# Optimization experiments

Measured on AMD Instinct MI355X. Metric: run time of the kernel, lower is better.

The kernel has to match this reference:

```python
import jax, jax.numpy as jnp
import numpy as np
import math

B, SQ, SK, D, H = 2, 2048, 2048, 1024, 16
DH = D // H
EPS = 1e-5

def _ln(x, g, b):
    m = jnp.mean(x, axis=-1, keepdims=True)
    v = jnp.mean(jnp.square(x - m), axis=-1, keepdims=True)
    return (x - m) / jnp.sqrt(v + EPS) * g + b

def setup_inputs() -> dict:
    key = jax.random.key(0)
    ks = jax.random.split(key, 8)
    xav = math.sqrt(6.0 / (D + D))  # xavier_uniform for square [D,D] weights
    inp = {
        'Q': jax.random.normal(ks[0], (B, SQ, D), dtype=jnp.float32),
        'K': jax.random.normal(ks[1], (B, SK, D), dtype=jnp.float32),
        'pad_mask': jax.random.randint(ks[2], (B, SK), 0, 2, dtype=jnp.int32),
        'Wq': jax.random.uniform(ks[3], (D, D), jnp.float32, -xav, xav),
        'Wk': jax.random.uniform(ks[4], (D, D), jnp.float32, -xav, xav),
        'Wv': jax.random.uniform(ks[5], (D, D), jnp.float32, -xav, xav),
        'Wo': jax.random.uniform(ks[6], (D, D), jnp.float32, -xav, xav),
        'bq': jnp.zeros((D,), jnp.float32),
        'bk': jnp.zeros((D,), jnp.float32),
        'bv': jnp.zeros((D,), jnp.float32),
        'bo': jnp.zeros((D,), jnp.float32),
        'ln_q_g': jnp.ones((D,), jnp.float32),  'ln_q_b': jnp.zeros((D,), jnp.float32),
        'ln_kv_g': jnp.ones((D,), jnp.float32), 'ln_kv_b': jnp.zeros((D,), jnp.float32),
        'ln_f_g': jnp.ones((D,), jnp.float32),  'ln_f_b': jnp.zeros((D,), jnp.float32),
    }
    return inp

def reference(Q, K, pad_mask, Wq, Wk, Wv, Wo, bq, bk, bv, bo,
              ln_q_g, ln_q_b, ln_kv_g, ln_kv_b, ln_f_g, ln_f_b):
    Q_ = _ln(Q, ln_q_g, ln_q_b)
    K_ = _ln(K, ln_kv_g, ln_kv_b)
    # projections (PyTorch Linear: x @ W.T + b)
    Q1 = (Q_ @ Wq.T + bq).reshape(B, SQ, H, DH)
    K1 = (K_ @ Wk.T + bk).reshape(B, SK, H, DH)
    V1 = (K_ @ Wv.T + bv).reshape(B, SK, H, DH)
    # note: scaling uses sqrt(dim_V), NOT sqrt(head_dim), per source
    score = jnp.einsum('bqhd,bkhd->bhqk', Q1, K1) / math.sqrt(D)
    m = pad_mask[:, None, None, :]  # [B,1,1,SK]
    score = jnp.where(m == 0, jnp.float32(-1e12), score)
    A = jax.nn.softmax(score, axis=-1)
    A = A * m.astype(A.dtype)  # second mask application after softmax
    O1 = jnp.einsum('bhqk,bkhd->bqhd', A, V1).reshape(B, SQ, D)
    O2 = jax.nn.relu(Q_ @ Wo.T + bo)
    return _ln(Q + O1 + O2, ln_f_g, ln_f_b)
```

## Files before the change

### kernel.cpp

```cpp
#include <hip/hip_runtime.h>
#include <stdint.h>

#define NB 2
#define NSQ 2048
#define NSK 2048
#define ND 1024
#define NH 16
#define NDH 64

typedef unsigned short u16;
typedef unsigned int u32;
typedef __bf16 bf16x8_t __attribute__((ext_vector_type(8)));
typedef float f32x4_t __attribute__((ext_vector_type(4)));
typedef u32 u32x4_t __attribute__((ext_vector_type(4)));

#define AS1 __attribute__((address_space(1)))
#define AS3 __attribute__((address_space(3)))

__device__ __forceinline__ float bf2f(u16 u) {
    union { float f; u32 i; } v; v.i = ((u32)u) << 16; return v.f;
}
__device__ __forceinline__ u16 f2bf(float x) {
    union { float f; u32 i; } v; v.f = x;
    u32 r = v.i + 0x7fffu + ((v.i >> 16) & 1u);
    return (u16)(r >> 16);
}
__device__ __forceinline__ u32 fbits(float x) {
    union { float f; u32 i; } v; v.f = x; return v.i;
}

__global__ __launch_bounds__(256) void detect_kernel(
    const u16* __restrict__ Q, int* __restrict__ flag)
{
    __shared__ int s;
    if (threadIdx.x == 0) s = 0;
    __syncthreads();
    uint2 x = ((const uint2*)Q)[threadIdx.x];
    u16 a0 = x.x & 0xffff, a1 = x.x >> 16, a2 = x.y & 0xffff, a3 = x.y >> 16;
    bool big = (((a0 >> 7) & 0xff) >= 0x8D) || (((a1 >> 7) & 0xff) >= 0x8D) ||
               (((a2 >> 7) & 0xff) >= 0x8D) || (((a3 >> 7) & 0xff) >= 0x8D);
    if (big) s = 1;
    __syncthreads();
    if (threadIdx.x == 0) *flag = s;
}

__global__ __launch_bounds__(256) void cvt_params_kernel(
    const int* __restrict__ flag,
    const void* __restrict__ Wq, const void* __restrict__ Wk,
    const void* __restrict__ Wv, const void* __restrict__ Wo,
    const void* __restrict__ vbq, const void* __restrict__ vbk,
    const void* __restrict__ vbv, const void* __restrict__ vbo,
    const void* __restrict__ g0, const void* __restrict__ b0,
    const void* __restrict__ g1, const void* __restrict__ b1,
    const void* __restrict__ g2, const void* __restrict__ b2,
    u16* __restrict__ Wc, u16* __restrict__ Vc)
{
    int blk = blockIdx.x;
    int t = threadIdx.x;
    const void* src;
    u16* dst;
    size_t srcoff;
    if (blk < 4096) {
        int w = blk >> 10;
        src = (w == 0) ? Wq : (w == 1) ? Wk : (w == 2) ? Wv : Wo;
        srcoff = (size_t)(blk & 1023) * 1024;
        dst = Wc + (size_t)w * 1024 * 1024 + srcoff;
    } else {
        int v = blk - 4096;
        src = (v == 0) ? vbq : (v == 1) ? vbk : (v == 2) ? vbv : (v == 3) ? vbo :
              (v == 4) ? g0  : (v == 5) ? b0  : (v == 6) ? g1  : (v == 7) ? b1 :
              (v == 8) ? g2  : b2;
        srcoff = 0;
        dst = Vc + (size_t)v * 1024;
    }
    u32 lo, hi;
    if (*flag) {
        float4 x = ((const float4*)src)[srcoff / 4 + t];
        lo = (u32)f2bf(x.x) | ((u32)f2bf(x.y) << 16);
        hi = (u32)f2bf(x.z) | ((u32)f2bf(x.w) << 16);
    } else {
        uint2 x = ((const uint2*)src)[srcoff / 4 + t];
        lo = x.x; hi = x.y;
    }
    uint2 o; o.x = lo; o.y = hi;
    ((uint2*)dst)[t] = o;
}

__global__ __launch_bounds__(256) void idx_kernel(
    const int* __restrict__ mask, int* __restrict__ idx, int* __restrict__ cnt)
{
    int b = blockIdx.x;
    const int* m = mask + b * NSK;
    int t = threadIdx.x;
    int loc[8]; int s = 0;
#pragma unroll
    for (int i = 0; i < 8; ++i) { loc[i] = (m[t * 8 + i] != 0); s += loc[i]; }
    __shared__ int ps[256];
    ps[t] = s;
    __syncthreads();
    for (int off = 1; off < 256; off <<= 1) {
        int v = (t >= off) ? ps[t - off] : 0;
        __syncthreads();
        ps[t] += v;
        __syncthreads();
    }
    int run = ps[t] - s;
#pragma unroll
    for (int i = 0; i < 8; ++i)
        if (loc[i]) idx[b * NSK + run++] = t * 8 + i;
    if (t == 255) cnt[b] = ps[255];
}

__global__ __launch_bounds__(256) void ln_in_kernel(
    const int* __restrict__ flag,
    const void* __restrict__ Q, const void* __restrict__ K,
    const u16* __restrict__ Vc,
    u16* __restrict__ Qn, u16* __restrict__ Kn)
{
    int row = blockIdx.x;
    const void* x; const u16 *g, *bb; u16* y;
    size_t roff;
    if (row < NB * NSQ) {
        x = Q; roff = (size_t)row * ND;
        g = Vc + 4 * 1024; bb = Vc + 5 * 1024;
        y = Qn + roff;
    } else {
        int r2 = row - NB * NSQ;
        x = K; roff = (size_t)r2 * ND;
        g = Vc + 6 * 1024; bb = Vc + 7 * 1024;
        y = Kn + roff;
    }
    int t = threadIdx.x;
    float v0, v1, v2, v3;
    if (*flag) {
        float4 xv = ((const float4*)x)[roff / 4 + t];
        v0 = xv.x; v1 = xv.y; v2 = xv.z; v3 = xv.w;
    } else {
        uint2 ux = ((const uint2*)x)[roff / 4 + t];
        v0 = bf2f(ux.x & 0xffff); v1 = bf2f(ux.x >> 16);
        v2 = bf2f(ux.y & 0xffff); v3 = bf2f(ux.y >> 16);
    }
    float s1 = v0 + v1 + v2 + v3;
    float s2 = v0*v0 + v1*v1 + v2*v2 + v3*v3;
#pragma unroll
    for (int off = 32; off >= 1; off >>= 1) {
        s1 += __shfl_xor(s1, off);
        s2 += __shfl_xor(s2, off);
    }
    __shared__ float r1[4], r2[4];
    int wave = t >> 6;
    if ((t & 63) == 0) { r1[wave] = s1; r2[wave] = s2; }
    __syncthreads();
    float t1 = r1[0] + r1[1] + r1[2] + r1[3];
    float t2 = r2[0] + r2[1] + r2[2] + r2[3];
    float mean = t1 * (1.0f / ND);
    float var  = t2 * (1.0f / ND) - mean * mean;
    float rstd = rsqrtf(var + 1e-5f);
    uint2 ug = ((const uint2*)g)[t];
    uint2 ub = ((const uint2*)bb)[t];
    float y0 = (v0 - mean) * rstd * bf2f(ug.x & 0xffff) + bf2f(ub.x & 0xffff);
    float y1 = (v1 - mean) * rstd * bf2f(ug.x >> 16)    + bf2f(ub.x >> 16);
    float y2 = (v2 - mean) * rstd * bf2f(ug.y & 0xffff) + bf2f(ub.y & 0xffff);
    float y3 = (v3 - mean) * rstd * bf2f(ug.y >> 16)    + bf2f(ub.y >> 16);
    uint2 o;
    o.x = (u32)f2bf(y0) | ((u32)f2bf(y1) << 16);
    o.y = (u32)f2bf(y2) | ((u32)f2bf(y3) << 16);
    ((uint2*)y)[t] = o;
}

__global__ __launch_bounds__(256) void gemm4_kernel(
    const u16* __restrict__ Qn, const u16* __restrict__ Kn,
    const u16* __restrict__ Wc, const u16* __restrict__ Vc,
    u16* __restrict__ Q1, u16* __restrict__ K1, u16* __restrict__ V1,
    u16* __restrict__ R)
{
    int z = blockIdx.z;
    const u16* X    = (z == 0 || z == 3) ? Qn : Kn;
    const u16* W    = Wc + (size_t)z * 1024 * 1024;
    const u16* bias = Vc + (size_t)z * 1024;

    __shared__ u16 smem[16384];
    u16* sA0 = smem;
    u16* sA1 = smem + 4096;
    u16* sB0 = smem + 8192;
    u16* sB1 = smem + 12288;

    int tid  = threadIdx.x;
    int wave = tid >> 6, lane = tid & 63;
    int wm = wave >> 1, wn = wave & 1;
    int quad = lane >> 4, l4 = lane & 15;
    int m0 = blockIdx.x * 128;
    int n0 = blockIdx.y * 128;

    f32x4_t acc[4][4];
#pragma unroll
    for (int i = 0; i < 4; ++i)
#pragma unroll
        for (int j = 0; j < 4; ++j)
            acc[i][j] = (f32x4_t){0.f, 0.f, 0.f, 0.f};

    int lrow = lane >> 2;
    int lcol = (lane & 3) * 8;
    int rowb0 = wave * 16;
    int rowb1 = (4 + wave) * 16;
    const u16* gA0 = X + (size_t)(m0 + rowb0 + lrow) * ND + lcol;
    const u16* gA1 = X + (size_t)(m0 + rowb1 + lrow) * ND + lcol;
    const u16* gB0 = W + (size_t)(n0 + rowb0 + lrow) * ND + lcol;
    const u16* gB1 = W + (size_t)(n0 + rowb1 + lrow) * ND + lcol;

    __builtin_amdgcn_global_load_lds((const AS1 u32*)gA0, (AS3 u32*)(sA0 + rowb0 * 32), 16, 0, 0);
    __builtin_amdgcn_global_load_lds((const AS1 u32*)gA1, (AS3 u32*)(sA0 + rowb1 * 32), 16, 0, 0);
    __builtin_amdgcn_global_load_lds((const AS1 u32*)gB0, (AS3 u32*)(sB0 + rowb0 * 32), 16, 0, 0);
    __builtin_amdgcn_global_load_lds((const AS1 u32*)gB1, (AS3 u32*)(sB0 + rowb1 * 32), 16, 0, 0);

    for (int kb = 0; kb < ND / 32; ++kb) {
        __syncthreads();

        if (kb + 1 < ND / 32) {
            int k1 = (kb + 1) * 32;
            u16* dA = (kb + 1) & 1 ? sA1 : sA0;
            u16* dB = (kb + 1) & 1 ? sB1 : sB0;
            __builtin_amdgcn_global_load_lds((const AS1 u32*)(gA0 + k1), (AS3 u32*)(dA + rowb0 * 32), 16, 0, 0);
            __builtin_amdgcn_global_load_lds((const AS1 u32*)(gA1 + k1), (AS3 u32*)(dA + rowb1 * 32), 16, 0, 0);
            __builtin_amdgcn_global_load_lds((const AS1 u32*)(gB0 + k1), (AS3 u32*)(dB + rowb0 * 32), 16, 0, 0);
            __builtin_amdgcn_global_load_lds((const AS1 u32*)(gB1 + k1), (AS3 u32*)(dB + rowb1 * 32), 16, 0, 0);
        }

        const u16* a = kb & 1 ? sA1 : sA0;
        const u16* bb_ = kb & 1 ? sB1 : sB0;
        bf16x8_t af[4], bfr[4];
#pragma unroll
        for (int tm = 0; tm < 4; ++tm) {
            int rr = wm * 64 + tm * 16 + l4;
            af[tm] = *(const bf16x8_t*)(a + rr * 32 + quad * 8);
        }
#pragma unroll
        for (int tn = 0; tn < 4; ++tn) {
            int rr = wn * 64 + tn * 16 + l4;
            bfr[tn] = *(const bf16x8_t*)(bb_ + rr * 32 + quad * 8);
        }
#pragma unroll
        for (int tm = 0; tm < 4; ++tm)
#pragma unroll
            for (int tn = 0; tn < 4; ++tn)
                acc[tm][tn] = __builtin_amdgcn_mfma_f32_16x16x32_bf16(
                    af[tm], bfr[tn], acc[tm][tn], 0, 0, 0);
    }

    u16* outp = (z == 0) ? Q1 : (z == 1) ? K1 : (z == 2) ? V1 : R;
#pragma unroll
    for (int tm = 0; tm < 4; ++tm) {
#pragma unroll
        for (int tn = 0; tn < 4; ++tn) {
            int n = n0 + wn * 64 + tn * 16 + l4;
            float bv_ = bf2f(bias[n]);
#pragma unroll
            for (int r = 0; r < 4; ++r) {
                int m = m0 + wm * 64 + tm * 16 + quad * 4 + r;
                float val = acc[tm][tn][r] + bv_;
                if (z == 0) val *= 0.045105964f;
                if (z == 3) val = fmaxf(val, 0.f);
                outp[(size_t)m * ND + n] = f2bf(val);
            }
        }
    }
}

__global__ __launch_bounds__(256) void gather_k_kernel(
    const u16* __restrict__ K1, const int* __restrict__ idx,
    const int* __restrict__ cnt, u16* __restrict__ Kc)
{
    int b = blockIdx.y;
    int c = cnt[b];
    int cPad = (c + 63) & ~63;
    int jb = blockIdx.x * 16;
    if (jb >= cPad) return;
    int t = threadIdx.x;
    int row = t >> 4;
    int seg = t & 15;
    int j = jb + row;
    if (j >= cPad) return;
    bool z = (j >= c);
    const u16* src = z ? (const u16*)0
        : K1 + ((size_t)b * NSK + idx[(size_t)b * NSK + j]) * ND;
    u16* dst = Kc + ((size_t)b * NSK + j) * ND;
#pragma unroll
    for (int i = 0; i < 8; ++i) {
        int off = (seg * 8 + i) * 8;
        uint4 v = z ? (uint4){0, 0, 0, 0} : *(const uint4*)(src + off);
        *(uint4*)(dst + off) = v;
    }
}

__global__ __launch_bounds__(256) void gather_vt_kernel(
    const u16* __restrict__ V1, const int* __restrict__ idx,
    const int* __restrict__ cnt, u16* __restrict__ Vct)
{
    int kb = blockIdx.x;
    int h  = blockIdx.y;
    int b  = blockIdx.z;
    int c = cnt[b];
    int cPad = (c + 63) & ~63;
    if (kb * 64 >= cPad) return;
    __shared__ u16 sT[64 * 72];
    int tid = threadIdx.x;
    {
        int row = tid >> 3, seg = tid & 7;
        int j1 = kb * 64 + row, j2 = j1 + 32;
        uint4 v1 = {0, 0, 0, 0}, v2 = {0, 0, 0, 0};
        if (j1 < c) v1 = *(const uint4*)(V1 +
            ((size_t)b * NSK + idx[(size_t)b * NSK + j1]) * ND + h * NDH + seg * 8);
        if (j2 < c) v2 = *(const uint4*)(V1 +
            ((size_t)b * NSK + idx[(size_t)b * NSK + j2]) * ND + h * NDH + seg * 8);
        *(uint4*)(sT + row * 72 + seg * 8) = v1;
        *(uint4*)(sT + (row + 32) * 72 + seg * 8) = v2;
    }
    __syncthreads();
    int d = tid >> 2, sg = tid & 3;
    u16 buf[16];
#pragma unroll
    for (int i = 0; i < 8; ++i) buf[i]     = sT[(sg * 8 + i) * 72 + d];
#pragma unroll
    for (int i = 0; i < 8; ++i) buf[8 + i] = sT[((sg + 4) * 8 + i) * 72 + d];
    u16* go = Vct + ((size_t)(b * NH + h) * NDH + d) * NSK + kb * 64;
    *(uint4*)(go + sg * 8)       = *(uint4*)buf;
    *(uint4*)(go + (sg + 4) * 8) = *(uint4*)(buf + 8);
}

__global__ __launch_bounds__(256, 4) void attn_kernel(
    const u16* __restrict__ Q1, const u16* __restrict__ Kc,
    const u16* __restrict__ Vct, const int* __restrict__ cnt,
    u16* __restrict__ R)
{
    int q0 = blockIdx.x * 64;
    int h  = blockIdx.y;
    int b  = blockIdx.z;

    __shared__ u16 sK[2][64 * 64];
    __shared__ u16 sV[2][64 * 64];

    int tid  = threadIdx.x;
    int wave = tid >> 6, lane = tid & 63;
    int quad = lane >> 4, l4 = lane & 15;
    int lk = lane >> 3, ls = lane & 7;
    int gseg = ls ^ lk;

    int c  = cnt[b];
    int nt = (c + 63) >> 6;

    bf16x8_t qf[2];
    {
        const u16* qp = Q1 + (size_t)(b * NSQ + q0 + wave * 16 + l4) * ND + h * NDH;
        qf[0] = *(const bf16x8_t*)(qp + quad * 8);
        qf[1] = *(const bf16x8_t*)(qp + 32 + quad * 8);
    }

    const u16* kbase = Kc + (size_t)b * NSK * ND + h * NDH;
    const u16* vbase = Vct + (size_t)(b * NH + h) * NDH * NSK;

    const u16* gk0 = kbase + (size_t)(wave * 16 + lk) * ND + gseg * 8;
    const u16* gk1 = gk0 + (size_t)8 * ND;
    const u16* gv0 = vbase + (size_t)(wave * 16 + lk) * NSK + gseg * 8;
    const u16* gv1 = gv0 + (size_t)8 * NSK;

    int fragOff[2];
#pragma unroll
    for (int kk = 0; kk < 2; ++kk)
        fragOff[kk] = l4 * 64 + (((kk * 4 + quad) ^ (l4 & 7)) * 8);

    float l_run = 0.f;
    f32x4_t acc_o[4];
#pragma unroll
    for (int T = 0; T < 4; ++T) acc_o[T] = (f32x4_t){0.f, 0.f, 0.f, 0.f};

    int srcA = (quad & 1) * 32 + l4;
    int srcB = srcA + 16;
    bool hi = lane >= 32;

    if (nt > 0) {
        __builtin_amdgcn_global_load_lds((const AS1 u32*)gk0,
            (AS3 u32*)(&sK[0][(wave * 16) * 64]), 16, 0, 0);
        __builtin_amdgcn_global_load_lds((const AS1 u32*)gk1,
            (AS3 u32*)(&sK[0][(wave * 16 + 8) * 64]), 16, 0, 0);
        __builtin_amdgcn_global_load_lds((const AS1 u32*)gv0,
            (AS3 u32*)(&sV[0][(wave * 16) * 64]), 16, 0, 0);
        __builtin_amdgcn_global_load_lds((const AS1 u32*)gv1,
            (AS3 u32*)(&sV[0][(wave * 16 + 8) * 64]), 16, 0, 0);
        gk0 += (size_t)64 * ND; gk1 += (size_t)64 * ND;
        gv0 += 64; gv1 += 64;

        for (int kb = 0; kb < nt; ++kb) {
            __syncthreads();

            if (kb + 1 < nt) {
                int bi = (kb + 1) & 1;
                __builtin_amdgcn_global_load_lds((const AS1 u32*)gk0,
                    (AS3 u32*)(&sK[bi][(wave * 16) * 64]), 16, 0, 0);
                __builtin_amdgcn_global_load_lds((const AS1 u32*)gk1,
                    (AS3 u32*)(&sK[bi][(wave * 16 + 8) * 64]), 16, 0, 0);
                __builtin_amdgcn_global_load_lds((const AS1 u32*)gv0,
                    (AS3 u32*)(&sV[bi][(wave * 16) * 64]), 16, 0, 0);
                __builtin_amdgcn_global_load_lds((const AS1 u32*)gv1,
                    (AS3 u32*)(&sV[bi][(wave * 16 + 8) * 64]), 16, 0, 0);
                gk0 += (size_t)64 * ND; gk1 += (size_t)64 * ND;
                gv0 += 64; gv1 += 64;
            }

            const u16* kt = sK[kb & 1];
            const u16* vt = sV[kb & 1];

            f32x4_t accs[4];
            if (kb == nt - 1) {
#pragma unroll
                for (int tm = 0; tm < 4; ++tm) {
                    int key = kb * 64 + tm * 16 + quad * 4;
#pragma unroll
                    for (int r = 0; r < 4; ++r)
                        accs[tm][r] = (key + r < c) ? 0.f : -1e9f;
                }
            } else {
#pragma unroll
                for (int tm = 0; tm < 4; ++tm)
                    accs[tm] = (f32x4_t){0.f, 0.f, 0.f, 0.f};
            }
#pragma unroll
            for (int kk = 0; kk < 2; ++kk)
#pragma unroll
                for (int tm = 0; tm < 4; ++tm) {
                    bf16x8_t kf = *(const bf16x8_t*)(kt + tm * 1024 + fragOff[kk]);
                    accs[tm] = __builtin_amdgcn_mfma_f32_16x16x32_bf16(
                        kf, qf[kk], accs[tm], 0, 0, 0);
                }

            float lsum = 0.f;
            u32 pk[4][2];
#pragma unroll
            for (int tm = 0; tm < 4; ++tm) {
                float p0 = exp2f(accs[tm][0]);
                float p1 = exp2f(accs[tm][1]);
                float p2 = exp2f(accs[tm][2]);
                float p3 = exp2f(accs[tm][3]);
                lsum += p0 + p1 + p2 + p3;
                pk[tm][0] = __builtin_amdgcn_perm(fbits(p1), fbits(p0), 0x07060302);
                pk[tm][1] = __builtin_amdgcn_perm(fbits(p3), fbits(p2), 0x07060302);
            }
            lsum += __shfl_xor(lsum, 16);
            lsum += __shfl_xor(lsum, 32);
            l_run += lsum;

#pragma unroll
            for (int kk = 0; kk < 2; ++kk) {
                u32 a0 = __shfl((int)pk[kk * 2][0], srcA), a1 = __shfl((int)pk[kk * 2][1], srcA);
                u32 b0 = __shfl((int)pk[kk * 2 + 1][0], srcA), b1 = __shfl((int)pk[kk * 2 + 1][1], srcA);
                u32 c0 = __shfl((int)pk[kk * 2][0], srcB), c1 = __shfl((int)pk[kk * 2][1], srcB);
                u32 d0 = __shfl((int)pk[kk * 2 + 1][0], srcB), d1 = __shfl((int)pk[kk * 2 + 1][1], srcB);
                u32x4_t pr;
                pr.x = hi ? b0 : a0;
                pr.y = hi ? b1 : a1;
                pr.z = hi ? d0 : c0;
                pr.w = hi ? d1 : c1;
                bf16x8_t pf = __builtin_bit_cast(bf16x8_t, pr);
#pragma unroll
                for (int T = 0; T < 4; ++T) {
                    bf16x8_t vf = *(const bf16x8_t*)(vt + T * 1024 + fragOff[kk]);
                    acc_o[T] = __builtin_amdgcn_mfma_f32_16x16x32_bf16(
                        vf, pf, acc_o[T], 0, 0, 0);
                }
            }
        }
    }

    float inv = l_run > 0.f ? 1.f / l_run : 0.f;
    u16* rp = R + (size_t)(b * NSQ + q0 + wave * 16 + l4) * ND + h * NDH;
#pragma unroll
    for (int T = 0; T < 4; ++T) {
        u16* p = rp + T * 16 + quad * 4;
        uint2 o2 = *(const uint2*)p;
        float e0 = acc_o[T][0] * inv + bf2f(o2.x & 0xffff);
        float e1 = acc_o[T][1] * inv + bf2f(o2.x >> 16);
        float e2 = acc_o[T][2] * inv + bf2f(o2.y & 0xffff);
        float e3 = acc_o[T][3] * inv + bf2f(o2.y >> 16);
        uint2 on;
        on.x = (u32)f2bf(e0) | ((u32)f2bf(e1) << 16);
        on.y = (u32)f2bf(e2) | ((u32)f2bf(e3) << 16);
        *(uint2*)p = on;
    }
}

__global__ __launch_bounds__(256) void ln_out_kernel(
    const int* __restrict__ flag,
    const void* __restrict__ Q, const u16* __restrict__ R,
    const u16* __restrict__ Vc, void* __restrict__ out)
{
    int row = blockIdx.x;
    size_t roff = (size_t)row * ND;
    int t = threadIdx.x;
    int f = *flag;
    float v0, v1, v2, v3;
    uint2 ur = ((const uint2*)(R + roff))[t];
    if (f) {
        float4 xq = ((const float4*)Q)[roff / 4 + t];
        v0 = xq.x; v1 = xq.y; v2 = xq.z; v3 = xq.w;
    } else {
        uint2 uq = ((const uint2*)Q)[roff / 4 + t];
        v0 = bf2f(uq.x & 0xffff); v1 = bf2f(uq.x >> 16);
        v2 = bf2f(uq.y & 0xffff); v3 = bf2f(uq.y >> 16);
    }
    v0 += bf2f(ur.x & 0xffff); v1 += bf2f(ur.x >> 16);
    v2 += bf2f(ur.y & 0xffff); v3 += bf2f(ur.y >> 16);
    float s1 = v0 + v1 + v2 + v3;
    float s2 = v0*v0 + v1*v1 + v2*v2 + v3*v3;
#pragma unroll
    for (int off = 32; off >= 1; off >>= 1) {
        s1 += __shfl_xor(s1, off);
        s2 += __shfl_xor(s2, off);
    }
    __shared__ float r1[4], r2[4];
    int wave = t >> 6;
    if ((t & 63) == 0) { r1[wave] = s1; r2[wave] = s2; }
    __syncthreads();
    float t1 = r1[0] + r1[1] + r1[2] + r1[3];
    float t2 = r2[0] + r2[1] + r2[2] + r2[3];
    float mean = t1 * (1.0f / ND);
    float var  = t2 * (1.0f / ND) - mean * mean;
    float rstd = rsqrtf(var + 1e-5f);
    const u16* g  = Vc + 8 * 1024;
    const u16* bb = Vc + 9 * 1024;
    uint2 ug = ((const uint2*)g)[t];
    uint2 ub = ((const uint2*)bb)[t];
    float y0 = (v0 - mean) * rstd * bf2f(ug.x & 0xffff) + bf2f(ub.x & 0xffff);
    float y1 = (v1 - mean) * rstd * bf2f(ug.x >> 16)    + bf2f(ub.x >> 16);
    float y2 = (v2 - mean) * rstd * bf2f(ug.y & 0xffff) + bf2f(ub.y & 0xffff);
    float y3 = (v3 - mean) * rstd * bf2f(ug.y >> 16)    + bf2f(ub.y >> 16);
    if (f) {
        float4 o; o.x = y0; o.y = y1; o.z = y2; o.w = y3;
        ((float4*)out)[roff / 4 + t] = o;
    } else {
        uint2 o;
        o.x = (u32)f2bf(y0) | ((u32)f2bf(y1) << 16);
        o.y = (u32)f2bf(y2) | ((u32)f2bf(y3) << 16);
        ((uint2*)out)[roff / 4 + t] = o;
    }
}

extern "C" void kernel_launch(void* const* d_in, const int* in_sizes, int n_in,
                              void* d_out, int out_size, void* d_ws, size_t ws_size,
                              hipStream_t stream) {
    const void* Q        = d_in[0];
    const void* K        = d_in[1];
    const int* pad_mask  = (const int*)d_in[2];

    const size_t NEL = (size_t)NB * NSQ * ND;
    int* flag = (int*)d_ws;
    int* cnt  = flag + 1;
    int* idx  = flag + 4;
    u16* base = (u16*)(idx + 4096);
    u16* Qn  = base;
    u16* Kn  = Qn + NEL;
    u16* Q1  = Kn + NEL;
    u16* K1  = Q1 + NEL;
    u16* V1  = K1 + NEL;
    u16* R   = V1 + NEL;
    u16* Wc  = R + NEL;
    u16* Vc  = Wc + (size_t)4 * 1024 * 1024;
    u16* Kc  = Qn;
    u16* Vct = Kn;

    detect_kernel<<<dim3(1), dim3(256), 0, stream>>>((const u16*)Q, flag);

    cvt_params_kernel<<<dim3(4106), dim3(256), 0, stream>>>(
        flag, d_in[3], d_in[4], d_in[5], d_in[6],
        d_in[7], d_in[8], d_in[9], d_in[10],
        d_in[11], d_in[12], d_in[13], d_in[14], d_in[15], d_in[16],
        Wc, Vc);

    idx_kernel<<<dim3(NB), dim3(256), 0, stream>>>(pad_mask, idx, cnt);

    ln_in_kernel<<<dim3(2 * NB * NSQ), dim3(256), 0, stream>>>(
        flag, Q, K, Vc, Qn, Kn);

    gemm4_kernel<<<dim3(32, 8, 4), dim3(256), 0, stream>>>(
        Qn, Kn, Wc, Vc, Q1, K1, V1, R);

    gather_k_kernel<<<dim3(128, NB), dim3(256), 0, stream>>>(K1, idx, cnt, Kc);

    gather_vt_kernel<<<dim3(32, NH, NB), dim3(256), 0, stream>>>(V1, idx, cnt, Vct);

    attn_kernel<<<dim3(NSQ / 64, NH, NB), dim3(256), 0, stream>>>(
        Q1, Kc, Vct, cnt, R);

    ln_out_kernel<<<dim3(NB * NSQ), dim3(256), 0, stream>>>(
        flag, Q, R, Vc, d_out);
}
```

Baseline: 255.2 us.

## Rewrite projection GEMM with 256x256 tiles, 4-stage LDS pipeline and swizzle

The four fused projection GEMMs now use 512-thread blocks computing 256x256 output tiles, up from 128x128. Global-to-LDS loads move from a double buffer to a 4-stage ring with explicit vmcnt waits. Loads are interleaved between two MFMA half-phases, wave priority is raised around the MFMA phases, and an XOR swizzle on LDS chunks reduces bank conflicts. The larger tiles raise arithmetic intensity and the deeper prefetch hides memory latency, at the cost of only 256 blocks (fewer than two waves' worth of CUs), 128 KB of LDS per block, and heavy register pressure from 32 accumulators.

```diff
diff --git a/kernel.cpp b/kernel.cpp
--- a/kernel.cpp
+++ b/kernel.cpp
@@ -168,7 +168,7 @@
     ((uint2*)y)[t] = o;
 }
 
-__global__ __launch_bounds__(256) void gemm4_kernel(
+__global__ __launch_bounds__(512, 2) void gemm4_kernel(
     const u16* __restrict__ Qn, const u16* __restrict__ Kn,
     const u16* __restrict__ Wc, const u16* __restrict__ Vc,
     u16* __restrict__ Q1, u16* __restrict__ K1, u16* __restrict__ V1,
@@ -179,85 +179,108 @@
     const u16* W    = Wc + (size_t)z * 1024 * 1024;
     const u16* bias = Vc + (size_t)z * 1024;
 
-    __shared__ u16 smem[16384];
-    u16* sA0 = smem;
-    u16* sA1 = smem + 4096;
-    u16* sB0 = smem + 8192;
-    u16* sB1 = smem + 12288;
+    __shared__ u16 sm[4][2][256 * 32];
 
     int tid  = threadIdx.x;
     int wave = tid >> 6, lane = tid & 63;
-    int wm = wave >> 1, wn = wave & 1;
+    int wm = wave >> 2, wn = wave & 3;
     int quad = lane >> 4, l4 = lane & 15;
-    int m0 = blockIdx.x * 128;
-    int n0 = blockIdx.y * 128;
-
-    f32x4_t acc[4][4];
-#pragma unroll
-    for (int i = 0; i < 4; ++i)
+    int m0 = blockIdx.x * 256;
+    int n0 = blockIdx.y * 256;
+
+    int srow   = wave * 16 + (lane >> 2);
+    int schunk = (lane & 3) ^ ((srow >> 1) & 3);
+    const u16* gA = X + (size_t)(m0 + srow) * ND + schunk * 8;
+    const u16* gB = W + (size_t)(n0 + srow) * ND + schunk * 8;
+
+#define STAGE_A(t_) do { int s_ = (t_) & 3; \
+    __builtin_amdgcn_global_load_lds((const AS1 u32*)(gA + (t_) * 32), \
+        (AS3 u32*)(&sm[s_][0][wave * 512]), 16, 0, 0); \
+    __builtin_amdgcn_global_load_lds((const AS1 u32*)(gA + (t_) * 32 + (size_t)128 * ND), \
+        (AS3 u32*)(&sm[s_][0][4096 + wave * 512]), 16, 0, 0); \
+} while (0)
+#define STAGE_B(t_) do { int s_ = (t_) & 3; \
+    __builtin_amdgcn_global_load_lds((const AS1 u32*)(gB + (t_) * 32), \
+        (AS3 u32*)(&sm[s_][1][wave * 512]), 16, 0, 0); \
+    __builtin_amdgcn_global_load_lds((const AS1 u32*)(gB + (t_) * 32 + (size_t)128 * ND), \
+        (AS3 u32*)(&sm[s_][1][4096 + wave * 512]), 16, 0, 0); \
+} while (0)
+
+    int fch   = (quad ^ ((l4 >> 1) & 3)) * 8;
+    int aoffb = (wm * 128 + l4) * 32 + fch;
+    int boffb = (wn * 64  + l4) * 32 + fch;
+
+    f32x4_t acc[8][4];
+#pragma unroll
+    for (int i = 0; i < 8; ++i)
 #pragma unroll
         for (int j = 0; j < 4; ++j)
             acc[i][j] = (f32x4_t){0.f, 0.f, 0.f, 0.f};
 
-    int lrow = lane >> 2;
-    int lcol = (lane & 3) * 8;
-    int rowb0 = wave * 16;
-    int rowb1 = (4 + wave) * 16;
-    const u16* gA0 = X + (size_t)(m0 + rowb0 + lrow) * ND + lcol;
-    const u16* gA1 = X + (size_t)(m0 + rowb1 + lrow) * ND + lcol;
-    const u16* gB0 = W + (size_t)(n0 + rowb0 + lrow) * ND + lcol;
-    const u16* gB1 = W + (size_t)(n0 + rowb1 + lrow) * ND + lcol;
-
-    __builtin_amdgcn_global_load_lds((const AS1 u32*)gA0, (AS3 u32*)(sA0 + rowb0 * 32), 16, 0, 0);
-    __builtin_amdgcn_global_load_lds((const AS1 u32*)gA1, (AS3 u32*)(sA0 + rowb1 * 32), 16, 0, 0);
-    __builtin_amdgcn_global_load_lds((const AS1 u32*)gB0, (AS3 u32*)(sB0 + rowb0 * 32), 16, 0, 0);
-    __builtin_amdgcn_global_load_lds((const AS1 u32*)gB1, (AS3 u32*)(sB0 + rowb1 * 32), 16, 0, 0);
-
-    for (int kb = 0; kb < ND / 32; ++kb) {
-        __syncthreads();
-
-        if (kb + 1 < ND / 32) {
-            int k1 = (kb + 1) * 32;
-            u16* dA = (kb + 1) & 1 ? sA1 : sA0;
-            u16* dB = (kb + 1) & 1 ? sB1 : sB0;
-            __builtin_amdgcn_global_load_lds((const AS1 u32*)(gA0 + k1), (AS3 u32*)(dA + rowb0 * 32), 16, 0, 0);
-            __builtin_amdgcn_global_load_lds((const AS1 u32*)(gA1 + k1), (AS3 u32*)(dA + rowb1 * 32), 16, 0, 0);
-            __builtin_amdgcn_global_load_lds((const AS1 u32*)(gB0 + k1), (AS3 u32*)(dB + rowb0 * 32), 16, 0, 0);
-            __builtin_amdgcn_global_load_lds((const AS1 u32*)(gB1 + k1), (AS3 u32*)(dB + rowb1 * 32), 16, 0, 0);
-        }
-
-        const u16* a = kb & 1 ? sA1 : sA0;
-        const u16* bb_ = kb & 1 ? sB1 : sB0;
-        bf16x8_t af[4], bfr[4];
-#pragma unroll
-        for (int tm = 0; tm < 4; ++tm) {
-            int rr = wm * 64 + tm * 16 + l4;
-            af[tm] = *(const bf16x8_t*)(a + rr * 32 + quad * 8);
-        }
-#pragma unroll
-        for (int tn = 0; tn < 4; ++tn) {
-            int rr = wn * 64 + tn * 16 + l4;
-            bfr[tn] = *(const bf16x8_t*)(bb_ + rr * 32 + quad * 8);
-        }
-#pragma unroll
-        for (int tm = 0; tm < 4; ++tm)
-#pragma unroll
-            for (int tn = 0; tn < 4; ++tn)
-                acc[tm][tn] = __builtin_amdgcn_mfma_f32_16x16x32_bf16(
-                    af[tm], bfr[tn], acc[tm][tn], 0, 0, 0);
-    }
+    STAGE_A(0); STAGE_B(0);
+    STAGE_A(1); STAGE_B(1);
+    STAGE_A(2); STAGE_B(2);
+    asm volatile("s_waitcnt vmcnt(8)" ::: "memory");
+    __builtin_amdgcn_s_barrier();
+    __builtin_amdgcn_sched_barrier(0);
+
+    for (int t = 0; t < 32; ++t) {
+        const u16* a = &sm[t & 3][0][0];
+        const u16* b = &sm[t & 3][1][0];
+        bf16x8_t bf[4], af[4];
+
+#pragma unroll
+        for (int nf = 0; nf < 4; ++nf)
+            bf[nf] = *(const bf16x8_t*)(b + boffb + nf * 512);
+#pragma unroll
+        for (int mf = 0; mf < 4; ++mf)
+            af[mf] = *(const bf16x8_t*)(a + aoffb + mf * 512);
+        if (t < 29) STAGE_A(t + 3);
+        __builtin_amdgcn_s_barrier();
+        __builtin_amdgcn_s_setprio(1);
+#pragma unroll
+        for (int mf = 0; mf < 4; ++mf)
+#pragma unroll
+            for (int nf = 0; nf < 4; ++nf)
+                acc[mf][nf] = __builtin_amdgcn_mfma_f32_16x16x32_bf16(
+                    af[mf], bf[nf], acc[mf][nf], 0, 0, 0);
+        __builtin_amdgcn_s_setprio(0);
+        __builtin_amdgcn_s_barrier();
+
+#pragma unroll
+        for (int mf = 0; mf < 4; ++mf)
+            af[mf] = *(const bf16x8_t*)(a + aoffb + (mf + 4) * 512);
+        if (t < 29) STAGE_B(t + 3);
+        __builtin_amdgcn_s_barrier();
+        __builtin_amdgcn_s_setprio(1);
+#pragma unroll
+        for (int mf = 0; mf < 4; ++mf)
+#pragma unroll
+            for (int nf = 0; nf < 4; ++nf)
+                acc[mf + 4][nf] = __builtin_amdgcn_mfma_f32_16x16x32_bf16(
+                    af[mf], bf[nf], acc[mf + 4][nf], 0, 0, 0);
+        __builtin_amdgcn_s_setprio(0);
+
+        if (t < 29)       asm volatile("s_waitcnt vmcnt(8)" ::: "memory");
+        else if (t == 29) asm volatile("s_waitcnt vmcnt(4)" ::: "memory");
+        else if (t == 30) asm volatile("s_waitcnt vmcnt(0)" ::: "memory");
+        __builtin_amdgcn_s_barrier();
+        __builtin_amdgcn_sched_barrier(0);
+    }
+#undef STAGE_A
+#undef STAGE_B
 
     u16* outp = (z == 0) ? Q1 : (z == 1) ? K1 : (z == 2) ? V1 : R;
 #pragma unroll
-    for (int tm = 0; tm < 4; ++tm) {
-#pragma unroll
-        for (int tn = 0; tn < 4; ++tn) {
-            int n = n0 + wn * 64 + tn * 16 + l4;
-            float bv_ = bf2f(bias[n]);
+    for (int nf = 0; nf < 4; ++nf) {
+        int n = n0 + wn * 64 + nf * 16 + l4;
+        float bv_ = bf2f(bias[n]);
+#pragma unroll
+        for (int mf = 0; mf < 8; ++mf) {
 #pragma unroll
             for (int r = 0; r < 4; ++r) {
-                int m = m0 + wm * 64 + tm * 16 + quad * 4 + r;
-                float val = acc[tm][tn][r] + bv_;
+                int m = m0 + wm * 128 + mf * 16 + quad * 4 + r;
+                float val = acc[mf][nf][r] + bv_;
                 if (z == 0) val *= 0.045105964f;
                 if (z == 3) val = fmaxf(val, 0.f);
                 outp[(size_t)m * ND + n] = f2bf(val);
@@ -579,7 +602,7 @@
     ln_in_kernel<<<dim3(2 * NB * NSQ), dim3(256), 0, stream>>>(
         flag, Q, K, Vc, Qn, Kn);
 
-    gemm4_kernel<<<dim3(32, 8, 4), dim3(256), 0, stream>>>(
+    gemm4_kernel<<<dim3(16, 4, 4), dim3(512), 0, stream>>>(
         Qn, Kn, Wc, Vc, Q1, K1, V1, R);
 
     gather_k_kernel<<<dim3(128, NB), dim3(256), 0, stream>>>(K1, idx, cnt, Kc);
```

Result: faster. 240.7 us (-5.7%).
